# Performance work log

Hardware: AMD Instinct MI355X
Metric: run time of the kernel (lower is better)

Reference implementation:

```python
import jax, jax.numpy as jnp
import numpy as np

UNITS = 1024
NUM_HEADS = 8


def setup_inputs() -> dict:
    key = jax.random.key(0)
    k1, k2, k3 = jax.random.split(key, 3)
    B, S = 8, 1024
    memory = jax.random.normal(k1, (B, S, 2 * UNITS), dtype=jnp.float32)
    query = jax.random.normal(k2, (B, S, UNITS), dtype=jnp.float32)
    seq_mask = jax.random.randint(k3, (B, S), 0, 2, dtype=jnp.int32)
    b = jnp.zeros((1,), dtype=jnp.float32)  # learned scalar bias added to logits
    return {"memory": memory, "query": query, "seq_mask": seq_mask, "b": b}


def _split_heads(x, n):
    # [B, S, D] -> [B, n, S, D//n]
    B, S, D = x.shape
    return x.reshape(B, S, n, D // n).transpose(0, 2, 1, 3)


def reference(memory, query, seq_mask, b):
    H = NUM_HEADS
    depth = UNITS // H
    Q = _split_heads(query, H) * (depth ** -0.5)          # [B,H,S,d]
    k_mem, v_mem = jnp.split(memory, 2, axis=2)
    K = _split_heads(k_mem, H)                            # [B,H,S,d]
    V = _split_heads(v_mem, H)                            # [B,H,S,d]
    logits = jnp.einsum('bhqd,bhkd->bhqk', Q, K) + b[0]   # [B,H,S,S]
    mask = seq_mask.astype(jnp.float32)[:, None, None, :]  # [B,1,1,S]
    logits = logits + (-1e30) * (1.0 - mask)
    weights = jax.nn.softmax(logits, axis=-1)
    out = jnp.einsum('bhqk,bhkd->bhqd', weights, V)       # [B,H,S,d]
    B, _, S, _ = out.shape
    return out.transpose(0, 2, 1, 3).reshape(B, S, UNITS)
```

## Files before the change

kernel.cpp:

```cpp
#include <hip/hip_runtime.h>
#include <stdint.h>


typedef __attribute__((ext_vector_type(8))) short bf16x8;
typedef __attribute__((ext_vector_type(4))) float f32x4;
typedef __attribute__((ext_vector_type(4))) unsigned int u32x4;

#define NB 8
#define SS 1024
#define NH 8
#define DH 128
#define BM 128
#define BN 64
#define KPAD 136
#define VPAD 72
#define PPAD 68

__device__ __forceinline__ unsigned short f2bf(float f) {
    unsigned int u = __builtin_bit_cast(unsigned int, f);
    u += 0x7fffu + ((u >> 16) & 1u);
    return (unsigned short)(u >> 16);
}

__device__ __forceinline__ unsigned int cvt_pk_bf16(float lo, float hi) {
#if __has_builtin(__builtin_amdgcn_cvt_pk_bf16_f32)
    typedef __attribute__((ext_vector_type(2))) __bf16 bf16x2_t;
    bf16x2_t r = __builtin_amdgcn_cvt_pk_bf16_f32(lo, hi);
    return __builtin_bit_cast(unsigned int, r);
#else
    return (unsigned int)f2bf(lo) | ((unsigned int)f2bf(hi) << 16);
#endif
}

__device__ __forceinline__ void bar_lgkm() {
    asm volatile("s_waitcnt lgkmcnt(0)" ::: "memory");
    __builtin_amdgcn_s_barrier();
    asm volatile("" ::: "memory");
}

__global__ __launch_bounds__(256, 2)
void attn_flash(const float* __restrict__ mem,
                const float* __restrict__ query,
                const int* __restrict__ seq_mask,
                float* __restrict__ out)
{
    __shared__ unsigned short K_lds[BN * KPAD];
    __shared__ unsigned short Vt_lds[DH * VPAD];
    __shared__ unsigned short P_lds[4 * 32 * PPAD];

    const int tid  = threadIdx.x;
    const int wave = tid >> 6;
    const int lane = tid & 63;
    const int g = lane >> 4;
    const int c = lane & 15;

    const int bh = blockIdx.x;
    const int b  = bh >> 3;
    const int h  = bh & 7;
    const int q0w = blockIdx.y * BM + wave * 32;

    bf16x8 qf[2][4];
    #pragma unroll
    for (int sub = 0; sub < 2; ++sub) {
        const float* qb = query + ((size_t)(b * SS + q0w + sub * 16 + c) << 10) + h * DH + g * 8;
        #pragma unroll
        for (int ks = 0; ks < 4; ++ks) {
            f32x4 lo = *(const f32x4*)(qb + ks * 32);
            f32x4 hi = *(const f32x4*)(qb + ks * 32 + 4);
            u32x4 q;
            q[0] = cvt_pk_bf16(lo[0], lo[1]);
            q[1] = cvt_pk_bf16(lo[2], lo[3]);
            q[2] = cvt_pk_bf16(hi[0], hi[1]);
            q[3] = cvt_pk_bf16(hi[2], hi[3]);
            qf[sub][ks] = __builtin_bit_cast(bf16x8, q);
        }
    }

    f32x4 acc[2][8];
    #pragma unroll
    for (int sub = 0; sub < 2; ++sub)
        #pragma unroll
        for (int i = 0; i < 8; ++i) acc[sub][i] = (f32x4){0.f, 0.f, 0.f, 0.f};
    float l_i[2][4] = {{0.f,0.f,0.f,0.f},{0.f,0.f,0.f,0.f}};

    const float cs = 0.12752789747141537f;

    const int krow = tid >> 4;
    const int kcc  = (tid & 15) * 8;
    const int vq   = tid & 31;
    const int vg8  = tid >> 5;

    const float* kbase = mem + ((size_t)(b * SS) << 11) + h * DH;
    const float* vbase = kbase + 1024;
    const int* mbase = seq_mask + b * SS;

    f32x4 pka[4], pkb[4];
    f32x4 pva0[2], pva1[2], pvb0[2], pvb1[2];
    int   pmsk[4];

    #pragma unroll
    for (int it = 0; it < 4; ++it) {
        const float* src = kbase + ((size_t)(it * 16 + krow) << 11) + kcc;
        pka[it] = *(const f32x4*)src;
        pkb[it] = *(const f32x4*)(src + 4);
    }
    #pragma unroll
    for (int task = 0; task < 2; ++task) {
        int d0 = vg8 * 8 + task * 64;
        const float* pa = vbase + ((size_t)(2 * vq) << 11) + d0;
        pva0[task] = *(const f32x4*)pa;
        pva1[task] = *(const f32x4*)(pa + 4);
        pvb0[task] = *(const f32x4*)(pa + 2048);
        pvb1[task] = *(const f32x4*)(pa + 2048 + 4);
    }
    #pragma unroll
    for (int j = 0; j < 4; ++j) pmsk[j] = mbase[j * 16 + c];

    for (int kt = 0; kt < SS / BN; ++kt) {
        const int kk0 = kt * BN;
        bar_lgkm();

        #pragma unroll
        for (int it = 0; it < 4; ++it) {
            u32x4 t;
            t[0] = cvt_pk_bf16(pka[it][0], pka[it][1]);
            t[1] = cvt_pk_bf16(pka[it][2], pka[it][3]);
            t[2] = cvt_pk_bf16(pkb[it][0], pkb[it][1]);
            t[3] = cvt_pk_bf16(pkb[it][2], pkb[it][3]);
            *(u32x4*)&K_lds[(it * 16 + krow) * KPAD + kcc] = t;
        }
        #pragma unroll
        for (int task = 0; task < 2; ++task) {
            int d0 = vg8 * 8 + task * 64;
            #pragma unroll
            for (int j = 0; j < 8; ++j) {
                float av = (j < 4) ? pva0[task][j] : pva1[task][j - 4];
                float bv = (j < 4) ? pvb0[task][j] : pvb1[task][j - 4];
                *(unsigned int*)&Vt_lds[(d0 + j) * VPAD + 2 * vq] =
                    cvt_pk_bf16(av, bv);
            }
        }
        float mb[4];
        #pragma unroll
        for (int j = 0; j < 4; ++j) mb[j] = pmsk[j] ? 0.f : -1e30f;

        const int kkn = (kt < SS / BN - 1) ? kk0 + BN : kk0;
        #pragma unroll
        for (int it = 0; it < 4; ++it) {
            const float* src = kbase + ((size_t)(kkn + it * 16 + krow) << 11) + kcc;
            pka[it] = *(const f32x4*)src;
            pkb[it] = *(const f32x4*)(src + 4);
        }
        #pragma unroll
        for (int task = 0; task < 2; ++task) {
            int d0 = vg8 * 8 + task * 64;
            const float* pa = vbase + ((size_t)(kkn + 2 * vq) << 11) + d0;
            pva0[task] = *(const f32x4*)pa;
            pva1[task] = *(const f32x4*)(pa + 4);
            pvb0[task] = *(const f32x4*)(pa + 2048);
            pvb1[task] = *(const f32x4*)(pa + 2048 + 4);
        }
        #pragma unroll
        for (int j = 0; j < 4; ++j) pmsk[j] = mbase[kkn + j * 16 + c];

        bar_lgkm();

        f32x4 s[2][4];
        #pragma unroll
        for (int sub = 0; sub < 2; ++sub)
            #pragma unroll
            for (int j = 0; j < 4; ++j) s[sub][j] = (f32x4){0.f, 0.f, 0.f, 0.f};
        #pragma unroll
        for (int ks = 0; ks < 4; ++ks) {
            #pragma unroll
            for (int j = 0; j < 4; ++j) {
                bf16x8 kf = *(const bf16x8*)&K_lds[(j * 16 + c) * KPAD + ks * 32 + g * 8];
                s[0][j] = __builtin_amdgcn_mfma_f32_16x16x32_bf16(qf[0][ks], kf, s[0][j], 0, 0, 0);
                s[1][j] = __builtin_amdgcn_mfma_f32_16x16x32_bf16(qf[1][ks], kf, s[1][j], 0, 0, 0);
            }
        }

        float p[2][4][4];
        #pragma unroll
        for (int sub = 0; sub < 2; ++sub)
            #pragma unroll
            for (int j = 0; j < 4; ++j)
                #pragma unroll
                for (int r = 0; r < 4; ++r) {
                    float pv = __builtin_amdgcn_exp2f(s[sub][j][r] * cs + mb[j]);
                    p[sub][j][r] = pv;
                    l_i[sub][r] += pv;
                }

        unsigned short* pw = &P_lds[wave * 32 * PPAD];
        #pragma unroll
        for (int sub = 0; sub < 2; ++sub)
            #pragma unroll
            for (int j = 0; j < 4; ++j) {
                #pragma unroll
                for (int rp = 0; rp < 2; ++rp) {
                    unsigned int w = cvt_pk_bf16(p[sub][j][2 * rp], p[sub][j][2 * rp + 1]);
                    pw[(sub * 16 + 4 * g + 2 * rp)     * PPAD + j * 16 + c] = (unsigned short)w;
                    pw[(sub * 16 + 4 * g + 2 * rp + 1) * PPAD + j * 16 + c] = (unsigned short)(w >> 16);
                }
            }
        asm volatile("s_waitcnt lgkmcnt(0)" ::: "memory");

        #pragma unroll
        for (int ks = 0; ks < 2; ++ks) {
            bf16x8 ap0 = *(const bf16x8*)&pw[(c)      * PPAD + ks * 32 + g * 8];
            bf16x8 ap1 = *(const bf16x8*)&pw[(16 + c) * PPAD + ks * 32 + g * 8];
            #pragma unroll
            for (int dt = 0; dt < 8; ++dt) {
                bf16x8 bv = *(const bf16x8*)&Vt_lds[(dt * 16 + c) * VPAD + ks * 32 + g * 8];
                acc[0][dt] = __builtin_amdgcn_mfma_f32_16x16x32_bf16(ap0, bv, acc[0][dt], 0, 0, 0);
                acc[1][dt] = __builtin_amdgcn_mfma_f32_16x16x32_bf16(ap1, bv, acc[1][dt], 0, 0, 0);
            }
        }
    }

    #pragma unroll
    for (int sub = 0; sub < 2; ++sub) {
        float inv[4];
        #pragma unroll
        for (int r = 0; r < 4; ++r) {
            float lr = l_i[sub][r];
            lr += __shfl_xor(lr, 1);
            lr += __shfl_xor(lr, 2);
            lr += __shfl_xor(lr, 4);
            lr += __shfl_xor(lr, 8);
            inv[r] = 1.f / lr;
        }
        #pragma unroll
        for (int r = 0; r < 4; ++r) {
            float* ob = out + ((size_t)(b * SS + q0w + sub * 16 + 4 * g + r) << 10) + h * DH + c;
            #pragma unroll
            for (int dt = 0; dt < 8; ++dt)
                ob[dt * 16] = acc[sub][dt][r] * inv[r];
        }
    }
}

extern "C" void kernel_launch(void* const* d_in, const int* in_sizes, int n_in,
                              void* d_out, int out_size, void* d_ws, size_t ws_size,
                              hipStream_t stream)
{
    (void)in_sizes; (void)n_in; (void)d_ws; (void)ws_size; (void)out_size;
    const float* mem    = (const float*)d_in[0];
    const float* query  = (const float*)d_in[1];
    const int* seq_mask = (const int*)d_in[2];
    dim3 grid(NB * NH, SS / BM);
    attn_flash<<<grid, 256, 0, stream>>>(mem, query, seq_mask, (float*)d_out);
}
```

Before: 186.9 us.

## Switch to 32x32x16 MFMA with register-resident P via permlane swaps

Reworks the attention inner loop to use 32x32x16 bf16 MFMAs and computes S transposed (K as the A operand), so the softmax probabilities can be repacked in registers with permlane32 swaps and fed directly into the PV MFMA. This removes the P shared-memory buffer and its store/load round trip. Masking now comes from a ballot over the mask word instead of per-lane loads, and s_setprio is raised around MFMA blocks. The output normalisation uses cross-lane shuffles, and the fragment index mapping is intricate, so a layout mismatch would give wrong results.

```diff
diff --git a/kernel.cpp b/kernel.cpp
--- a/kernel.cpp
+++ b/kernel.cpp
@@ -4,6 +4,7 @@
 
 typedef __attribute__((ext_vector_type(8))) short bf16x8;
 typedef __attribute__((ext_vector_type(4))) float f32x4;
+typedef __attribute__((ext_vector_type(16))) float f32x16;
 typedef __attribute__((ext_vector_type(4))) unsigned int u32x4;
 
 #define NB 8
@@ -14,7 +15,6 @@
 #define BN 64
 #define KPAD 136
 #define VPAD 72
-#define PPAD 68
 
 __device__ __forceinline__ unsigned short f2bf(float f) {
     unsigned int u = __builtin_bit_cast(unsigned int, f);
@@ -38,6 +38,21 @@
     asm volatile("" ::: "memory");
 }
 
+__device__ __forceinline__ void pswap(unsigned int &a, unsigned int &b) {
+#if __has_builtin(__builtin_amdgcn_permlane32_swap)
+    auto r = __builtin_amdgcn_permlane32_swap(a, b, false, false);
+    a = (unsigned int)r[0];
+    b = (unsigned int)r[1];
+#else
+    unsigned int sa = (unsigned int)__shfl_xor((int)a, 32, 64);
+    unsigned int sb = (unsigned int)__shfl_xor((int)b, 32, 64);
+    const bool hh = (threadIdx.x & 32) != 0;
+    unsigned int na = hh ? sb : a;
+    unsigned int nb = hh ? b : sa;
+    a = na; b = nb;
+#endif
+}
+
 __global__ __launch_bounds__(256, 2)
 void attn_flash(const float* __restrict__ mem,
                 const float* __restrict__ query,
@@ -46,42 +61,40 @@
 {
     __shared__ unsigned short K_lds[BN * KPAD];
     __shared__ unsigned short Vt_lds[DH * VPAD];
-    __shared__ unsigned short P_lds[4 * 32 * PPAD];
 
     const int tid  = threadIdx.x;
     const int wave = tid >> 6;
     const int lane = tid & 63;
-    const int g = lane >> 4;
-    const int c = lane & 15;
+    const int hi   = lane >> 5;
+    const int l31  = lane & 31;
 
     const int bh = blockIdx.x;
     const int b  = bh >> 3;
     const int h  = bh & 7;
     const int q0w = blockIdx.y * BM + wave * 32;
 
-    bf16x8 qf[2][4];
-    #pragma unroll
-    for (int sub = 0; sub < 2; ++sub) {
-        const float* qb = query + ((size_t)(b * SS + q0w + sub * 16 + c) << 10) + h * DH + g * 8;
-        #pragma unroll
-        for (int ks = 0; ks < 4; ++ks) {
-            f32x4 lo = *(const f32x4*)(qb + ks * 32);
-            f32x4 hi = *(const f32x4*)(qb + ks * 32 + 4);
+    bf16x8 qf[8];
+    {
+        const float* qb = query + ((size_t)(b * SS + q0w + l31) << 10) + h * DH + hi * 8;
+        #pragma unroll
+        for (int dep = 0; dep < 8; ++dep) {
+            f32x4 lo = *(const f32x4*)(qb + dep * 16);
+            f32x4 ho = *(const f32x4*)(qb + dep * 16 + 4);
             u32x4 q;
             q[0] = cvt_pk_bf16(lo[0], lo[1]);
             q[1] = cvt_pk_bf16(lo[2], lo[3]);
-            q[2] = cvt_pk_bf16(hi[0], hi[1]);
-            q[3] = cvt_pk_bf16(hi[2], hi[3]);
-            qf[sub][ks] = __builtin_bit_cast(bf16x8, q);
-        }
-    }
-
-    f32x4 acc[2][8];
-    #pragma unroll
-    for (int sub = 0; sub < 2; ++sub)
-        #pragma unroll
-        for (int i = 0; i < 8; ++i) acc[sub][i] = (f32x4){0.f, 0.f, 0.f, 0.f};
-    float l_i[2][4] = {{0.f,0.f,0.f,0.f},{0.f,0.f,0.f,0.f}};
+            q[2] = cvt_pk_bf16(ho[0], ho[1]);
+            q[3] = cvt_pk_bf16(ho[2], ho[3]);
+            qf[dep] = __builtin_bit_cast(bf16x8, q);
+        }
+    }
+
+    f32x16 acc[4];
+    #pragma unroll
+    for (int dt = 0; dt < 4; ++dt)
+        #pragma unroll
+        for (int i = 0; i < 16; ++i) acc[dt][i] = 0.f;
+    float l_i = 0.f;
 
     const float cs = 0.12752789747141537f;
 
@@ -96,7 +109,6 @@
 
     f32x4 pka[4], pkb[4];
     f32x4 pva0[2], pva1[2], pvb0[2], pvb1[2];
-    int   pmsk[4];
 
     #pragma unroll
     for (int it = 0; it < 4; ++it) {
@@ -113,11 +125,12 @@
         pvb0[task] = *(const f32x4*)(pa + 2048);
         pvb1[task] = *(const f32x4*)(pa + 2048 + 4);
     }
-    #pragma unroll
-    for (int j = 0; j < 4; ++j) pmsk[j] = mbase[j * 16 + c];
 
     for (int kt = 0; kt < SS / BN; ++kt) {
         const int kk0 = kt * BN;
+
+        const int mv = mbase[kk0 + lane];
+
         bar_lgkm();
 
         #pragma unroll
@@ -140,9 +153,6 @@
                     cvt_pk_bf16(av, bv);
             }
         }
-        float mb[4];
-        #pragma unroll
-        for (int j = 0; j < 4; ++j) mb[j] = pmsk[j] ? 0.f : -1e30f;
 
         const int kkn = (kt < SS / BN - 1) ? kk0 + BN : kk0;
         #pragma unroll
@@ -160,84 +170,77 @@
             pvb0[task] = *(const f32x4*)(pa + 2048);
             pvb1[task] = *(const f32x4*)(pa + 2048 + 4);
         }
-        #pragma unroll
-        for (int j = 0; j < 4; ++j) pmsk[j] = mbase[kkn + j * 16 + c];
+
+        const unsigned long long bmask = __ballot(mv != 0);
+        const unsigned int wsh0 = (unsigned int)(bmask >> (4 * hi));
+        const unsigned int wsh1 = (unsigned int)(bmask >> (32 + 4 * hi));
 
         bar_lgkm();
 
-        f32x4 s[2][4];
-        #pragma unroll
-        for (int sub = 0; sub < 2; ++sub)
-            #pragma unroll
-            for (int j = 0; j < 4; ++j) s[sub][j] = (f32x4){0.f, 0.f, 0.f, 0.f};
-        #pragma unroll
-        for (int ks = 0; ks < 4; ++ks) {
-            #pragma unroll
-            for (int j = 0; j < 4; ++j) {
-                bf16x8 kf = *(const bf16x8*)&K_lds[(j * 16 + c) * KPAD + ks * 32 + g * 8];
-                s[0][j] = __builtin_amdgcn_mfma_f32_16x16x32_bf16(qf[0][ks], kf, s[0][j], 0, 0, 0);
-                s[1][j] = __builtin_amdgcn_mfma_f32_16x16x32_bf16(qf[1][ks], kf, s[1][j], 0, 0, 0);
-            }
-        }
-
-        float p[2][4][4];
-        #pragma unroll
-        for (int sub = 0; sub < 2; ++sub)
-            #pragma unroll
-            for (int j = 0; j < 4; ++j)
+        #pragma unroll
+        for (int jt = 0; jt < 2; ++jt) {
+            const unsigned int mword = jt ? wsh1 : wsh0;
+
+            f32x16 s;
+            #pragma unroll
+            for (int i = 0; i < 16; ++i) s[i] = 0.f;
+            __builtin_amdgcn_s_setprio(1);
+            #pragma unroll
+            for (int dep = 0; dep < 8; ++dep) {
+                bf16x8 kf = *(const bf16x8*)&K_lds[(jt * 32 + l31) * KPAD + dep * 16 + hi * 8];
+                s = __builtin_amdgcn_mfma_f32_32x32x16_bf16(kf, qf[dep], s, 0, 0, 0);
+            }
+            __builtin_amdgcn_s_setprio(0);
+
+            float p[16];
+            #pragma unroll
+            for (int r = 0; r < 16; ++r) {
+                const int sr = (r & 3) + 8 * (r >> 2);
+                float e = __builtin_amdgcn_exp2f(s[r] * cs);
+                float m = (float)((mword >> sr) & 1u);
+                p[r] = e * m;
+            }
+            {
+                float t0 = (p[0] + p[1]) + (p[2] + p[3]);
+                float t1 = (p[4] + p[5]) + (p[6] + p[7]);
+                float t2 = (p[8] + p[9]) + (p[10] + p[11]);
+                float t3 = (p[12] + p[13]) + (p[14] + p[15]);
+                l_i += (t0 + t1) + (t2 + t3);
+            }
+
+            unsigned int w[8];
+            #pragma unroll
+            for (int i = 0; i < 8; ++i) w[i] = cvt_pk_bf16(p[2 * i], p[2 * i + 1]);
+            pswap(w[0], w[2]); pswap(w[1], w[3]);
+            pswap(w[4], w[6]); pswap(w[5], w[7]);
+            bf16x8 af0 = __builtin_bit_cast(bf16x8, (u32x4){w[0], w[1], w[2], w[3]});
+            bf16x8 af1 = __builtin_bit_cast(bf16x8, (u32x4){w[4], w[5], w[6], w[7]});
+
+            __builtin_amdgcn_s_setprio(1);
+            #pragma unroll
+            for (int ksl = 0; ksl < 2; ++ksl) {
+                bf16x8 ap = ksl ? af1 : af0;
                 #pragma unroll
-                for (int r = 0; r < 4; ++r) {
-                    float pv = __builtin_amdgcn_exp2f(s[sub][j][r] * cs + mb[j]);
-                    p[sub][j][r] = pv;
-                    l_i[sub][r] += pv;
+                for (int dt = 0; dt < 4; ++dt) {
+                    bf16x8 bv = *(const bf16x8*)&Vt_lds[(dt * 32 + l31) * VPAD +
+                                                        jt * 32 + ksl * 16 + hi * 8];
+                    acc[dt] = __builtin_amdgcn_mfma_f32_32x32x16_bf16(ap, bv, acc[dt], 0, 0, 0);
                 }
-
-        unsigned short* pw = &P_lds[wave * 32 * PPAD];
-        #pragma unroll
-        for (int sub = 0; sub < 2; ++sub)
-            #pragma unroll
-            for (int j = 0; j < 4; ++j) {
-                #pragma unroll
-                for (int rp = 0; rp < 2; ++rp) {
-                    unsigned int w = cvt_pk_bf16(p[sub][j][2 * rp], p[sub][j][2 * rp + 1]);
-                    pw[(sub * 16 + 4 * g + 2 * rp)     * PPAD + j * 16 + c] = (unsigned short)w;
-                    pw[(sub * 16 + 4 * g + 2 * rp + 1) * PPAD + j * 16 + c] = (unsigned short)(w >> 16);
-                }
-            }
-        asm volatile("s_waitcnt lgkmcnt(0)" ::: "memory");
-
-        #pragma unroll
-        for (int ks = 0; ks < 2; ++ks) {
-            bf16x8 ap0 = *(const bf16x8*)&pw[(c)      * PPAD + ks * 32 + g * 8];
-            bf16x8 ap1 = *(const bf16x8*)&pw[(16 + c) * PPAD + ks * 32 + g * 8];
-            #pragma unroll
-            for (int dt = 0; dt < 8; ++dt) {
-                bf16x8 bv = *(const bf16x8*)&Vt_lds[(dt * 16 + c) * VPAD + ks * 32 + g * 8];
-                acc[0][dt] = __builtin_amdgcn_mfma_f32_16x16x32_bf16(ap0, bv, acc[0][dt], 0, 0, 0);
-                acc[1][dt] = __builtin_amdgcn_mfma_f32_16x16x32_bf16(ap1, bv, acc[1][dt], 0, 0, 0);
-            }
-        }
-    }
-
-    #pragma unroll
-    for (int sub = 0; sub < 2; ++sub) {
-        float inv[4];
-        #pragma unroll
-        for (int r = 0; r < 4; ++r) {
-            float lr = l_i[sub][r];
-            lr += __shfl_xor(lr, 1);
-            lr += __shfl_xor(lr, 2);
-            lr += __shfl_xor(lr, 4);
-            lr += __shfl_xor(lr, 8);
-            inv[r] = 1.f / lr;
-        }
-        #pragma unroll
-        for (int r = 0; r < 4; ++r) {
-            float* ob = out + ((size_t)(b * SS + q0w + sub * 16 + 4 * g + r) << 10) + h * DH + c;
-            #pragma unroll
-            for (int dt = 0; dt < 8; ++dt)
-                ob[dt * 16] = acc[sub][dt][r] * inv[r];
-        }
+            }
+            __builtin_amdgcn_s_setprio(0);
+        }
+    }
+
+    float lt = l_i + __shfl_xor(l_i, 32, 64);
+    float invl = 1.f / lt;
+    #pragma unroll
+    for (int r = 0; r < 16; ++r) {
+        const int qrow = (r & 3) + 8 * (r >> 2) + 4 * hi;
+        float iv = __shfl(invl, qrow, 64);
+        float* ob = out + ((size_t)(b * SS + q0w + qrow) << 10) + h * DH + l31;
+        #pragma unroll
+        for (int dt = 0; dt < 4; ++dt)
+            ob[dt * 32] = acc[dt][r] * iv;
     }
 }
 
```

New measurement: 174.2 us. 6.8% less time.
